# Performance work log

Measured on AMD Instinct MI355X. Metric: run time of the kernel, lower is better.

The kernel has to match this reference:

```python
import jax, jax.numpy as jnp
import numpy as np

D, ED, N, R, K, NL = 128, 256, 16, 8, 4, 3   # d_model, d_inner, d_state, dt_rank, d_conv, n_layers
B, L = 4, 1024
HID, OUT = 256, 2
EPS = 1e-5


def setup_inputs() -> dict:
    key = jax.random.key(0)
    ks = jax.random.split(key, 16)
    g = lambda k, shape, s=0.05: jax.random.normal(k, shape, dtype=jnp.float32) * s
    return {
        "x": jax.random.normal(ks[0], (B, L, D), dtype=jnp.float32),
        # Mamba params, stacked over (2 directions, NL layers)
        "rms_w": jnp.ones((2, NL, D), jnp.float32),
        "in_w": g(ks[1], (2, NL, 2 * ED, D)),
        "in_b": g(ks[2], (2, NL, 2 * ED)),
        "conv_w": g(ks[3], (2, NL, ED, K)),
        "conv_b": g(ks[4], (2, NL, ED)),
        "xproj_w": g(ks[5], (2, NL, R + 2 * N, ED)),
        "dt_w": g(ks[6], (2, NL, ED, R)),
        "dt_b": g(ks[7], (2, NL, ED)),
        "A_log": jnp.broadcast_to(jnp.log(jnp.arange(1.0, N + 1.0, dtype=jnp.float32)), (2, NL, ED, N)) + 0.0,
        "Dp": jnp.ones((2, NL, ED), jnp.float32),
        "out_w": g(ks[8], (2, NL, D, ED)),
        "out_b": g(ks[9], (2, NL, D)),
        # MLP head params (BatchNorm in training mode: batch stats)
        "bn1_g": jnp.ones((2 * D,), jnp.float32), "bn1_b": jnp.zeros((2 * D,), jnp.float32),
        "w1": g(ks[10], (HID, 2 * D)), "b1": g(ks[11], (HID,)),
        "bn2_g": jnp.ones((HID,), jnp.float32), "bn2_b": jnp.zeros((HID,), jnp.float32),
        "w2": g(ks[12], (HID, HID)), "b2": g(ks[13], (HID,)),
        "bn3_g": jnp.ones((HID,), jnp.float32), "bn3_b": jnp.zeros((HID,), jnp.float32),
        "w3": g(ks[14], (OUT, HID)), "b3": g(ks[15], (OUT,)),
    }


def _rms(x, w):
    return x * jax.lax.rsqrt(jnp.mean(x * x, axis=-1, keepdims=True) + EPS) * w


def _dwconv(x, w, b):
    # causal depthwise conv; x: (B,L,ED), w: (ED,K)
    y = jax.lax.conv_general_dilated(x.transpose(0, 2, 1), w[:, None, :], (1,), [(K - 1, 0)],
                                     feature_group_count=ED, dimension_numbers=("NCH", "OIH", "NCH"))
    return y.transpose(0, 2, 1) + b


def _ssm(dA, dBx, C):
    # dA,dBx: (B,L,ED,N); C: (B,L,N) -> y: (B,L,ED)
    def step(h, inp):
        a, bx, c = inp
        h = a * h + bx
        return h, jnp.einsum("ben,bn->be", h, c)
    h0 = jnp.zeros((dA.shape[0], ED, N), dA.dtype)
    _, ys = jax.lax.scan(step, h0, (dA.transpose(1, 0, 2, 3), dBx.transpose(1, 0, 2, 3), C.transpose(1, 0, 2)))
    return ys.transpose(1, 0, 2)


def _block(x, in_w, in_b, conv_w, conv_b, xproj_w, dt_w, dt_b, A_log, Dp, out_w, out_b):
    xz = x @ in_w.T + in_b
    xi, z = xz[..., :ED], xz[..., ED:]
    xi = jax.nn.silu(_dwconv(xi, conv_w, conv_b))
    dbc = xi @ xproj_w.T
    dt, Bm, Cm = dbc[..., :R], dbc[..., R:R + N], dbc[..., R + N:]
    delta = jax.nn.softplus(dt @ dt_w.T + dt_b)            # (B,L,ED)
    A = -jnp.exp(A_log)                                    # (ED,N)
    dA = jnp.exp(delta[..., None] * A)                     # (B,L,ED,N)
    dBx = (delta * xi)[..., None] * Bm[:, :, None, :]      # (B,L,ED,N)
    y = _ssm(dA, dBx, Cm) + Dp * xi
    y = y * jax.nn.silu(z)
    return y @ out_w.T + out_b


def _mamba(x, d, rms_w, in_w, in_b, conv_w, conv_b, xproj_w, dt_w, dt_b, A_log, Dp, out_w, out_b):
    for l in range(NL):
        x = x + _block(_rms(x, rms_w[d, l]), in_w[d, l], in_b[d, l], conv_w[d, l], conv_b[d, l],
                       xproj_w[d, l], dt_w[d, l], dt_b[d, l], A_log[d, l], Dp[d, l], out_w[d, l], out_b[d, l])
    return x


def _bn(x, g, b):
    m = jnp.mean(x, axis=0)
    v = jnp.mean((x - m) ** 2, axis=0)  # biased var, torch BN training mode
    return (x - m) * jax.lax.rsqrt(v + EPS) * g + b


def _forward(x, rms_w, in_w, in_b, conv_w, conv_b, xproj_w, dt_w, dt_b, A_log, Dp, out_w, out_b,
             bn1_g, bn1_b, w1, b1, bn2_g, bn2_b, w2, b2, bn3_g, bn3_b, w3, b3):
    mp = (rms_w, in_w, in_b, conv_w, conv_b, xproj_w, dt_w, dt_b, A_log, Dp, out_w, out_b)
    fwd = _mamba(x, 0, *mp)
    bwd = jnp.flip(_mamba(jnp.flip(x, axis=1), 1, *mp), axis=1)
    h = jnp.concatenate([fwd, bwd], axis=2).reshape(B * L, 2 * D)
    h = jax.nn.leaky_relu(_bn(h, bn1_g, bn1_b) @ w1.T + b1)
    h = jax.nn.leaky_relu(_bn(h, bn2_g, bn2_b) @ w2.T + b2)
    h = _bn(h, bn3_g, bn3_b) @ w3.T + b3
    return h.reshape(B, L, OUT)


def reference(x, rms_w, in_w, in_b, conv_w, conv_b, xproj_w, dt_w, dt_b, A_log, Dp, out_w, out_b,
              bn1_g, bn1_b, w1, b1, bn2_g, bn2_b, w2, b2, bn3_g, bn3_b, w3, b3):
    return _forward(x, rms_w, in_w, in_b, conv_w, conv_b, xproj_w, dt_w, dt_b, A_log, Dp, out_w, out_b,
                    bn1_g, bn1_b, w1, b1, bn2_g, bn2_b, w2, b2, bn3_g, bn3_b, w3, b3)
```

## Files before the change

### kernel.cpp

```cpp
#include <hip/hip_runtime.h>
#include <hip/hip_bf16.h>
#include <hip/hip_fp16.h>

#define NL 3
#define EPS 1e-5f

#define C_INB    393984L
#define C_CONVW  397056L
#define C_CONVB  403200L
#define C_XPROJW 404736L
#define C_DTW    466176L
#define C_DTB    478464L
#define C_ALOG   480000L
#define C_DP     504576L
#define C_OUTB   702720L
#define C_BN1G   703488L
#define C_BN1B   703744L
#define C_B1     769536L
#define C_BN2G   769792L
#define C_BN2B   770048L
#define C_B2     835840L
#define C_BN3G   836096L
#define C_BN3B   836352L
#define C_W3     836608L
#define C_B3     837120L
#define FLAG_OFF 837184L
#define X0_OFF   837248L
#define X1_OFF   1361536L
#define XZT_OFF  1885824L
#define DBCT_OFF 8177280L
#define YGP_OFF  8504960L
#define BNA_OFF  10603648L
#define HINW_OFF  10605184L
#define HOUTW_OFF 10801792L
#define HW1_OFF   10900096L
#define HW2_OFF   10932864L
#define HXW_OFF   10965632L
#define H1_OFF   XZT_OFF
#define H2_OFF   (XZT_OFF + 1048576L)

#define ASLD 68

struct Ptrs { const void* p[25]; };

typedef _Float16 half8 __attribute__((ext_vector_type(8)));
typedef float f32x4 __attribute__((ext_vector_type(4)));

static __device__ const int  CV_SRC[21] = {0,0,3,4,5,6,7,8,9,10,12,13,14,16,17,18,20,21,22,23,24};
static __device__ const long CV_DST[21] = {X0_OFF,X1_OFF,C_INB,C_CONVW,C_CONVB,C_XPROJW,C_DTW,C_DTB,C_ALOG,C_DP,
                                           C_OUTB,C_BN1G,C_BN1B,C_B1,C_BN2G,C_BN2B,C_B2,C_BN3G,C_BN3B,C_W3,C_B3};
static __device__ const int  CV_SZ[21]  = {524288,524288,3072,6144,1536,61440,12288,1536,24576,1536,
                                           768,256,256,256,256,256,256,256,256,512,2};

__device__ inline float ldsrc(const void* s, long i, bool isbf) {
  if (isbf) { unsigned int u = ((const unsigned short*)s)[i]; return __uint_as_float(u << 16); }
  return ((const float*)s)[i];
}

__global__ __launch_bounds__(256) void g_convert(Ptrs ps, float* __restrict__ ws) {
  bool isbf = (*(const unsigned int*)ps.p[1]) == 0x3F803F80u;
  int job = blockIdx.y;
  if (job == 0 && blockIdx.x == 0 && threadIdx.x == 0) ws[FLAG_OFF] = isbf ? 1.f : 0.f;
  int tid0 = blockIdx.x * 256 + threadIdx.x;
  int stride = gridDim.x * 256;
  if (job < 21) {
    int n = CV_SZ[job];
    const void* s = ps.p[CV_SRC[job]];
    float* dp = ws + CV_DST[job];
    bool permute = (job < 2);
    for (int i = tid0; i < n; i += stride) {
      long si = i;
      if (permute) {
        int row = i >> 7, col = i & 127;
        int b = row >> 10, p = row & 1023;
        int t = ((p & 63) << 4) + (p >> 6);
        si = ((long)((b << 10) + t) << 7) + col;
      }
      dp[i] = ldsrc(s, si, isbf);
    }
  } else if (job == 21) {
    _Float16* dp = (_Float16*)(ws + HINW_OFF);
    const void* sw = ps.p[2]; const void* sr = ps.p[1];
    for (int i = tid0; i < 393216; i += stride) {
      int dl = i >> 16, k = i & 127;
      dp[i] = (_Float16)(ldsrc(sw, i, isbf) * ldsrc(sr, dl*128 + k, isbf));
    }
  } else if (job == 22) {
    _Float16* dp = (_Float16*)(ws + HOUTW_OFF);
    const void* s = ps.p[11];
    for (int i = tid0; i < 196608; i += stride) dp[i] = (_Float16)ldsrc(s, i, isbf);
  } else if (job == 23) {
    _Float16* dp = (_Float16*)(ws + HW1_OFF);
    const void* s = ps.p[15];
    for (int i = tid0; i < 65536; i += stride) dp[i] = (_Float16)ldsrc(s, i, isbf);
  } else if (job == 24) {
    _Float16* dp = (_Float16*)(ws + HW2_OFF);
    const void* s = ps.p[19];
    for (int i = tid0; i < 65536; i += stride) dp[i] = (_Float16)ldsrc(s, i, isbf);
  } else if (job == 25) {
    for (int i = tid0; i < 1536; i += stride) ws[BNA_OFF + i] = 0.f;
  } else {
    _Float16* dp = (_Float16*)(ws + HXW_OFF);
    const void* s = ps.p[6];
    for (int i = tid0; i < 98304; i += stride) {
      int dl = i >> 14;
      int rem = i & 16383;
      int nn = rem >> 8, k = rem & 255;
      float v = (nn < 40) ? ldsrc(s, (long)(dl*40+nn)*256 + k, isbf) : 0.f;
      dp[i] = (_Float16)v;
    }
  }
}

__device__ inline void mm_inner(const float* As, const float* Bs, float4* acc) {
  int tx = threadIdx.x & 15, ty = threadIdx.x >> 4;
  #pragma unroll
  for (int k = 0; k < 64; ++k) {
    float4 av = *(const float4*)&As[k*ASLD + ty*4];
    float4 bv = *(const float4*)&Bs[k*ASLD + tx*4];
    acc[0].x = fmaf(av.x,bv.x,acc[0].x); acc[0].y = fmaf(av.x,bv.y,acc[0].y); acc[0].z = fmaf(av.x,bv.z,acc[0].z); acc[0].w = fmaf(av.x,bv.w,acc[0].w);
    acc[1].x = fmaf(av.y,bv.x,acc[1].x); acc[1].y = fmaf(av.y,bv.y,acc[1].y); acc[1].z = fmaf(av.y,bv.z,acc[1].z); acc[1].w = fmaf(av.y,bv.w,acc[1].w);
    acc[2].x = fmaf(av.z,bv.x,acc[2].x); acc[2].y = fmaf(av.z,bv.y,acc[2].y); acc[2].z = fmaf(av.z,bv.z,acc[2].z); acc[2].w = fmaf(av.z,bv.w,acc[2].w);
    acc[3].x = fmaf(av.w,bv.x,acc[3].x); acc[3].y = fmaf(av.w,bv.y,acc[3].y); acc[3].z = fmaf(av.w,bv.z,acc[3].z); acc[3].w = fmaf(av.w,bv.w,acc[3].w);
  }
}

__device__ inline void stageT_g(float* S, const float* src, int ld, int row0, int k0, int nvalid) {
  int m = threadIdx.x >> 2, q = threadIdx.x & 3;
  const float* p = src + (long)(row0 + m) * ld + k0 + q*16;
  bool ok = (row0 + m) < nvalid;
  #pragma unroll
  for (int j = 0; j < 4; ++j) {
    float4 v = ok ? *(const float4*)(p + j*4) : make_float4(0.f,0.f,0.f,0.f);
    int kk = q*16 + j*4;
    S[(kk+0)*ASLD+m] = v.x; S[(kk+1)*ASLD+m] = v.y; S[(kk+2)*ASLD+m] = v.z; S[(kk+3)*ASLD+m] = v.w;
  }
}

__device__ inline float softplusf(float x) {
  if (x > 20.f) return x;
  return __logf(1.f + __expf(x));
}
__device__ inline float siluf(float a) { return a / (1.f + __expf(-a)); }

__global__ __launch_bounds__(256) void g_k1m(float* __restrict__ ws, int layer) {
  int d = blockIdx.z, nt = blockIdx.y, pt = blockIdx.x;
  const float* X = ws + (d ? X1_OFF : X0_OFF);
  const _Float16* Wf = (const _Float16*)(ws + HINW_OFF) + (long)(d*NL+layer)*65536;
  const float* Bi = ws + C_INB + (d*NL+layer)*512;
  __shared__ float rsq[256];
  __shared__ float rsc[64];
  int p0 = pt*64;
  {
    int row = threadIdx.x >> 2, q = threadIdx.x & 3;
    const float* xp = X + (long)(p0+row)*128 + q*32;
    float s = 0.f;
    #pragma unroll
    for (int j = 0; j < 8; ++j) {
      float4 v = *(const float4*)(xp + j*4);
      s += v.x*v.x + v.y*v.y + v.z*v.z + v.w*v.w;
    }
    rsq[row*4+q] = s;
  }
  __syncthreads();
  if (threadIdx.x < 64) {
    float s = rsq[threadIdx.x*4] + rsq[threadIdx.x*4+1] + rsq[threadIdx.x*4+2] + rsq[threadIdx.x*4+3];
    rsc[threadIdx.x] = rsqrtf(s * (1.f/128.f) + EPS);
  }
  __syncthreads();
  int w = threadIdx.x >> 6, lane = threadIdx.x & 63;
  int quad = lane >> 4, lm = lane & 15;
  int n0 = nt*64 + w*16;
  f32x4 zero = {0.f,0.f,0.f,0.f};
  f32x4 acc[4] = {zero, zero, zero, zero};
  #pragma unroll
  for (int s = 0; s < 4; ++s) {
    int k0 = s*32 + quad*8;
    half8 af = *(const half8*)(Wf + (long)(n0+lm)*128 + k0);
    #pragma unroll
    for (int t = 0; t < 4; ++t) {
      int pr = t*16 + lm;
      const float* xp = X + (long)(p0+pr)*128 + k0;
      float4 v0 = *(const float4*)xp;
      float4 v1 = *(const float4*)(xp+4);
      float r = rsc[pr];
      half8 bf;
      bf[0]=(_Float16)(v0.x*r); bf[1]=(_Float16)(v0.y*r); bf[2]=(_Float16)(v0.z*r); bf[3]=(_Float16)(v0.w*r);
      bf[4]=(_Float16)(v1.x*r); bf[5]=(_Float16)(v1.y*r); bf[6]=(_Float16)(v1.z*r); bf[7]=(_Float16)(v1.w*r);
      acc[t] = __builtin_amdgcn_mfma_f32_16x16x32_f16(af, bf, acc[t], 0, 0, 0);
    }
  }
  float* xzt = ws + XZT_OFF + (long)d*2097152L;
  #pragma unroll
  for (int r = 0; r < 4; ++r) {
    int n = n0 + quad*4 + r;
    float bias = Bi[n];
    #pragma unroll
    for (int t = 0; t < 4; ++t) {
      int p = p0 + t*16 + lm;
      xzt[(long)n*4096 + p] = acc[t][r] + bias;
    }
  }
}

#define AHLD 264
__global__ __launch_bounds__(256) void g_k3m(float* __restrict__ ws, int layer) {
  int d = blockIdx.z, b = blockIdx.y;
  int ii = blockIdx.x >> 2, c0 = (blockIdx.x & 3) * 16;
  const float* xz = ws + XZT_OFF + (long)d*2097152L;
  const float* cw = ws + C_CONVW + (long)(d*NL+layer)*1024;
  const float* cbp = ws + C_CONVB + (d*NL+layer)*256;
  const _Float16* Wx = (const _Float16*)(ws + HXW_OFF) + (long)(d*NL+layer)*16384;
  __shared__ __align__(16) _Float16 Ah[16*AHLD];
  int col[4], sh[4];
  col[0] = ii; sh[0] = 0;
  #pragma unroll
  for (int j = 1; j < 4; ++j) {
    if (d == 0) { if (ii-j >= 0) { col[j]=ii-j; sh[j]=0; } else { col[j]=ii-j+16; sh[j]=-1; } }
    else        { if (ii+j <= 15){ col[j]=ii+j; sh[j]=0; } else { col[j]=ii+j-16; sh[j]=1; } }
  }
  int c = threadIdx.x & 15, eh = threadIdx.x >> 4;
  int gc = c0 + c;
  long rowbase = (long)b*1024;
  #pragma unroll 4
  for (int r = 0; r < 16; ++r) {
    int e = eh*16 + r;
    const float* xrow = xz + (long)e*4096 + rowbase;
    float4 cwv = *(const float4*)(cw + e*4);
    float v0 = xrow[col[0]*64 + gc];
    bool b1 = (sh[1] < 0 && gc == 0) || (sh[1] > 0 && gc == 63);
    bool b2 = (sh[2] < 0 && gc == 0) || (sh[2] > 0 && gc == 63);
    bool b3 = (sh[3] < 0 && gc == 0) || (sh[3] > 0 && gc == 63);
    float v1 = b1 ? 0.f : xrow[col[1]*64 + gc + sh[1]];
    float v2 = b2 ? 0.f : xrow[col[2]*64 + gc + sh[2]];
    float v3 = b3 ? 0.f : xrow[col[3]*64 + gc + sh[3]];
    float a = cbp[e] + cwv.w*v0 + cwv.z*v1 + cwv.y*v2 + cwv.x*v3;
    Ah[c*AHLD + e] = (_Float16)siluf(a);
  }
  __syncthreads();
  int w = threadIdx.x >> 6, lane = threadIdx.x & 63;
  int quad = lane >> 4, lm = lane & 15;
  f32x4 acc = {0.f,0.f,0.f,0.f};
  #pragma unroll
  for (int s = 0; s < 8; ++s) {
    int k0 = s*32 + quad*8;
    half8 af = *(const half8*)(Wx + (long)(w*16+lm)*256 + k0);
    half8 bf = *(const half8*)(&Ah[lm*AHLD + k0]);
    acc = __builtin_amdgcn_mfma_f32_16x16x32_f16(af, bf, acc, 0, 0, 0);
  }
  float* dbcT = ws + DBCT_OFF + (long)d*163840L;
  long P0 = (long)b*1024 + ii*64 + c0;
  #pragma unroll
  for (int r = 0; r < 4; ++r) {
    int n = w*16 + quad*4 + r;
    if (n < 40) dbcT[(long)n*4096 + P0 + lm] = acc[r];
  }
}

__global__ __launch_bounds__(256) void g_k5c(float* __restrict__ ws, int layer) {
  int d = blockIdx.z, b = blockIdx.y, eg = blockIdx.x;
  int es = threadIdx.x >> 6;
  int c  = threadIdx.x & 63;
  int e = eg*4 + es;
  int g0 = b*1024 + c;
  const float* xzrow = ws + XZT_OFF + (long)d*2097152L + (long)e*4096 + g0;
  const float* zp    = ws + XZT_OFF + (long)d*2097152L + (long)(256+e)*4096 + g0;
  const float* dbc = ws + DBCT_OFF + (long)d*163840L + g0;
  float*       yo  = ws + YGP_OFF + (long)d*1048576L + (long)e*4096 + g0;
  const float* dw = ws + C_DTW + (long)((d*NL+layer)*256 + e)*8;
  float dtb = ws[C_DTB + (d*NL+layer)*256 + e];
  const float* al = ws + C_ALOG + (long)((d*NL+layer)*256 + e)*16;
  float Dpe = ws[C_DP + (d*NL+layer)*256 + e];
  float4 cwv = *(const float4*)(ws + C_CONVW + (long)((d*NL+layer)*256 + e)*4);
  float cb = ws[C_CONVB + (d*NL+layer)*256 + e];
  float dtw[8];
  #pragma unroll
  for (int n = 0; n < 8; ++n) dtw[n] = dw[n];
  float Anv[16]; bool fast = true;
  #pragma unroll
  for (int n = 0; n < 16; ++n) {
    Anv[n] = -__expf(al[n]);
    fast = fast && (fabsf(Anv[n] + (float)(n+1)) < 1e-3f * (float)(n+1));
  }
  float w1, w2, w3;
  if (d == 0) {
    if (c > 0) { w1 = xzrow[959]; w2 = xzrow[895]; w3 = xzrow[831]; }
    else { w1 = w2 = w3 = 0.f; }
  } else {
    if (c < 63) { w1 = xzrow[1]; w2 = xzrow[65]; w3 = xzrow[129]; }
    else { w1 = w2 = w3 = 0.f; }
  }
  __shared__ float aL[4*64*17];
  __shared__ float hL[4*64*17];
  float h[16], ap[16], del[16], xcv[16];
  float Q = 1.f;
  #pragma unroll
  for (int n = 0; n < 16; ++n) { h[n] = 0.f; ap[n] = 1.f; }
  int i0 = d ? 15 : 0, di = d ? -1 : 1;
  for (int s = 0; s < 16; ++s) {
    int i = i0 + s*di;
    int off = i*64;
    float a0 = dtb;
    #pragma unroll
    for (int n = 0; n < 8; ++n) a0 += dbc[(long)n*4096 + off] * dtw[n];
    float dl = softplusf(a0);
    float xt = xzrow[off];
    float xc = siluf(cb + cwv.w*xt + cwv.z*w1 + cwv.y*w2 + cwv.x*w3);
    w3 = w2; w2 = w1; w1 = xt;
    del[s] = dl; xcv[s] = xc;
    float dx = dl * xc;
    if (fast) {
      float q = __expf(-dl);
      float qp[16];
      qp[0]=q; qp[1]=q*q; qp[2]=qp[1]*q; qp[3]=qp[1]*qp[1];
      float q4=qp[3];
      qp[4]=qp[0]*q4; qp[5]=qp[1]*q4; qp[6]=qp[2]*q4; qp[7]=q4*q4;
      float q8=qp[7];
      #pragma unroll
      for (int j = 0; j < 8; ++j) qp[8+j]=qp[j]*q8;
      Q *= q;
      #pragma unroll
      for (int n = 0; n < 16; ++n)
        h[n] = fmaf(qp[n], h[n], dx * dbc[(long)(8+n)*4096 + off]);
    } else {
      #pragma unroll
      for (int n = 0; n < 16; ++n) {
        float a = __expf(dl * Anv[n]);
        ap[n] *= a;
        h[n] = fmaf(a, h[n], dx * dbc[(long)(8+n)*4096 + off]);
      }
    }
  }
  if (fast) {
    float p = Q;
    #pragma unroll
    for (int n = 0; n < 16; ++n) { ap[n] = p; p *= Q; }
  }
  int base = (es*64 + c)*17;
  #pragma unroll
  for (int n = 0; n < 16; ++n) { aL[base+n] = ap[n]; hL[base+n] = h[n]; }
  __syncthreads();
  if (threadIdx.x < 64) {
    int e2 = threadIdx.x >> 4, n = threadIdx.x & 15;
    float h0 = 0.f;
    for (int s2 = 0; s2 < 64; ++s2) {
      int cc = d ? (63 - s2) : s2;
      int ix = (e2*64 + cc)*17 + n;
      float ta = aL[ix], th = hL[ix];
      aL[ix] = h0;
      h0 = fmaf(ta, h0, th);
    }
  }
  __syncthreads();
  #pragma unroll
  for (int n = 0; n < 16; ++n) h[n] = aL[base+n];
  for (int s = 0; s < 16; ++s) {
    int i = i0 + s*di;
    int off = i*64;
    float dl = del[s], xc = xcv[s];
    float dx = dl * xc;
    float zr = zp[off];
    float zg = zr / (1.f + __expf(-zr));
    float ya[4] = {0.f,0.f,0.f,0.f};
    if (fast) {
      float q = __expf(-dl);
      float qp[16];
      qp[0]=q; qp[1]=q*q; qp[2]=qp[1]*q; qp[3]=qp[1]*qp[1];
      float q4=qp[3];
      qp[4]=qp[0]*q4; qp[5]=qp[1]*q4; qp[6]=qp[2]*q4; qp[7]=q4*q4;
      float q8=qp[7];
      #pragma unroll
      for (int j = 0; j < 8; ++j) qp[8+j]=qp[j]*q8;
      #pragma unroll
      for (int n = 0; n < 16; ++n) {
        h[n] = fmaf(qp[n], h[n], dx * dbc[(long)(8+n)*4096 + off]);
        ya[n & 3] = fmaf(h[n], dbc[(long)(24+n)*4096 + off], ya[n & 3]);
      }
    } else {
      #pragma unroll
      for (int n = 0; n < 16; ++n) {
        float a = __expf(dl * Anv[n]);
        h[n] = fmaf(a, h[n], dx * dbc[(long)(8+n)*4096 + off]);
        ya[n & 3] = fmaf(h[n], dbc[(long)(24+n)*4096 + off], ya[n & 3]);
      }
    }
    float y = (ya[0] + ya[1]) + (ya[2] + ya[3]);
    y = fmaf(Dpe, xc, y);
    yo[off] = y * zg;
  }
}

__global__ __launch_bounds__(256) void g_k61(float* __restrict__ ws, int layer) {
  int d = blockIdx.z, pt = blockIdx.x;
  int p0 = pt*16;
  const float* Y = ws + YGP_OFF + (long)d*1048576L;
  const _Float16* Wf = (const _Float16*)(ws + HOUTW_OFF) + (long)(d*NL+layer)*32768;
  const float* Ob = ws + C_OUTB + (d*NL+layer)*128;
  float* Xd = ws + (d ? X1_OFF : X0_OFF);
  __shared__ __align__(16) _Float16 Ah[16*264];
  __shared__ float Xn[16*137];
  __shared__ float rsq[64];
  __shared__ float rsc[16];
  {
    int e = threadIdx.x;
    const float* yp = Y + (long)e*4096 + p0;
    float4 v0 = *(const float4*)yp;
    float4 v1 = *(const float4*)(yp+4);
    float4 v2 = *(const float4*)(yp+8);
    float4 v3 = *(const float4*)(yp+12);
    float vv[16] = {v0.x,v0.y,v0.z,v0.w, v1.x,v1.y,v1.z,v1.w,
                    v2.x,v2.y,v2.z,v2.w, v3.x,v3.y,v3.z,v3.w};
    #pragma unroll
    for (int p = 0; p < 16; ++p) Ah[p*264 + e] = (_Float16)vv[p];
  }
  __syncthreads();
  int w = threadIdx.x >> 6, lane = threadIdx.x & 63;
  int quad = lane >> 4, lm = lane & 15;
  f32x4 zero = {0.f,0.f,0.f,0.f};
  f32x4 acc[2] = {zero, zero};
  #pragma unroll
  for (int s = 0; s < 8; ++s) {
    int k0 = s*32 + quad*8;
    half8 af = *(const half8*)(&Ah[lm*264 + k0]);
    #pragma unroll
    for (int t = 0; t < 2; ++t) {
      int n = w*32 + t*16 + lm;
      half8 bf = *(const half8*)(Wf + (long)n*256 + k0);
      acc[t] = __builtin_amdgcn_mfma_f32_16x16x32_f16(af, bf, acc[t], 0, 0, 0);
    }
  }
  bool dostats = (layer == NL-1);
  float* bna = ws + BNA_OFF;
  #pragma unroll
  for (int t = 0; t < 2; ++t) {
    int n = w*32 + t*16 + lm;
    float ob = Ob[n];
    float s1 = 0.f, s2 = 0.f;
    #pragma unroll
    for (int r = 0; r < 4; ++r) {
      int p = p0 + quad*4 + r;
      float v = acc[t][r] + ob + Xd[(long)p*128 + n];
      Xd[(long)p*128 + n] = v;
      Xn[(quad*4 + r)*137 + n] = v;
      s1 += v; s2 += v*v;
    }
    if (dostats) {
      s1 += __shfl_xor(s1, 16, 64); s2 += __shfl_xor(s2, 16, 64);
      s1 += __shfl_xor(s1, 32, 64); s2 += __shfl_xor(s2, 32, 64);
      if (quad == 0) {
        int ch = d*128 + n;
        atomicAdd(&bna[ch], s1);
        atomicAdd(&bna[256 + ch], s2);
      }
    }
  }
  if (layer == NL-1) return;
  __syncthreads();
  if (threadIdx.x < 64) {
    int pl = threadIdx.x >> 2, qq = threadIdx.x & 3;
    float s = 0.f;
    const float* xr = &Xn[pl*137 + qq*32];
    #pragma unroll
    for (int k = 0; k < 32; ++k) s += xr[k]*xr[k];
    rsq[threadIdx.x] = s;
  }
  __syncthreads();
  if (threadIdx.x < 16) {
    float s = rsq[threadIdx.x*4] + rsq[threadIdx.x*4+1] + rsq[threadIdx.x*4+2] + rsq[threadIdx.x*4+3];
    rsc[threadIdx.x] = rsqrtf(s * (1.f/128.f) + EPS);
  }
  __syncthreads();
  const _Float16* Wn = (const _Float16*)(ws + HINW_OFF) + (long)(d*NL+layer+1)*65536;
  const float* Bi = ws + C_INB + (d*NL+layer+1)*512;
  f32x4 acc2[8] = {zero,zero,zero,zero,zero,zero,zero,zero};
  float r = rsc[lm];
  #pragma unroll
  for (int s = 0; s < 4; ++s) {
    int k0 = s*32 + quad*8;
    half8 bf;
    const float* xr = &Xn[lm*137 + k0];
    #pragma unroll
    for (int j = 0; j < 8; ++j) bf[j] = (_Float16)(xr[j] * r);
    #pragma unroll
    for (int tt = 0; tt < 8; ++tt) {
      int n2 = w*128 + tt*16 + lm;
      half8 af = *(const half8*)(Wn + (long)n2*128 + k0);
      acc2[tt] = __builtin_amdgcn_mfma_f32_16x16x32_f16(af, bf, acc2[tt], 0, 0, 0);
    }
  }
  float* xzt = ws + XZT_OFF + (long)d*2097152L;
  #pragma unroll
  for (int tt = 0; tt < 8; ++tt) {
    #pragma unroll
    for (int rr = 0; rr < 4; ++rr) {
      int n2 = w*128 + tt*16 + quad*4 + rr;
      xzt[(long)n2*4096 + p0 + lm] = acc2[tt][rr] + Bi[n2];
    }
  }
}

template<int STAGE>
__global__ __launch_bounds__(256) void g_hgm(float* __restrict__ ws) {
  int p0 = blockIdx.x * 16;
  __shared__ float scL[256], shL[256];
  {
    int k = threadIdx.x;
    float S = ws[BNA_OFF + STAGE*512 + k], S2 = ws[BNA_OFF + STAGE*512 + 256 + k];
    float mean = S * (1.f/4096.f);
    float var = S2 * (1.f/4096.f) - mean*mean;
    const float* g = ws + (STAGE == 0 ? C_BN1G : C_BN2G);
    const float* bb = ws + (STAGE == 0 ? C_BN1B : C_BN2B);
    float sc = g[k] * rsqrtf(var + EPS);
    scL[k] = sc; shL[k] = bb[k] - mean*sc;
  }
  __syncthreads();
  const _Float16* Wf = (const _Float16*)(ws + (STAGE == 0 ? HW1_OFF : HW2_OFF));
  const float* bias = ws + (STAGE == 0 ? C_B1 : C_B2);
  float* H = ws + (STAGE == 0 ? H1_OFF : H2_OFF);
  int w = threadIdx.x >> 6, lane = threadIdx.x & 63;
  int quad = lane >> 4, lm = lane & 15;
  f32x4 zero = {0.f,0.f,0.f,0.f};
  f32x4 acc[4] = {zero, zero, zero, zero};
  #pragma unroll
  for (int s = 0; s < 8; ++s) {
    int k0 = s*32 + quad*8;
    const float* src;
    if (STAGE == 0) src = (k0 < 128) ? (ws + X0_OFF + (long)(p0+lm)*128 + k0)
                                     : (ws + X1_OFF + (long)(p0+lm)*128 + (k0-128));
    else            src = ws + H1_OFF + (long)(p0+lm)*256 + k0;
    float4 v0 = *(const float4*)src, v1 = *(const float4*)(src+4);
    float4 c0 = *(const float4*)&scL[k0], c1 = *(const float4*)&scL[k0+4];
    float4 h0 = *(const float4*)&shL[k0], h1 = *(const float4*)&shL[k0+4];
    half8 af;
    af[0]=(_Float16)(v0.x*c0.x+h0.x); af[1]=(_Float16)(v0.y*c0.y+h0.y);
    af[2]=(_Float16)(v0.z*c0.z+h0.z); af[3]=(_Float16)(v0.w*c0.w+h0.w);
    af[4]=(_Float16)(v1.x*c1.x+h1.x); af[5]=(_Float16)(v1.y*c1.y+h1.y);
    af[6]=(_Float16)(v1.z*c1.z+h1.z); af[7]=(_Float16)(v1.w*c1.w+h1.w);
    #pragma unroll
    for (int t = 0; t < 4; ++t) {
      int n = w*64 + t*16 + lm;
      half8 bf = *(const half8*)(Wf + (long)n*256 + k0);
      acc[t] = __builtin_amdgcn_mfma_f32_16x16x32_f16(af, bf, acc[t], 0, 0, 0);
    }
  }
  float* bna = ws + BNA_OFF + (STAGE+1)*512;
  #pragma unroll
  for (int t = 0; t < 4; ++t) {
    int n = w*64 + t*16 + lm;
    float bs = bias[n];
    float s1 = 0.f, s2 = 0.f;
    #pragma unroll
    for (int r = 0; r < 4; ++r) {
      int p = p0 + quad*4 + r;
      float v = acc[t][r] + bs;
      v = v > 0.f ? v : 0.01f*v;
      H[(long)p*256 + n] = v;
      s1 += v; s2 += v*v;
    }
    s1 += __shfl_xor(s1, 16, 64); s2 += __shfl_xor(s2, 16, 64);
    s1 += __shfl_xor(s1, 32, 64); s2 += __shfl_xor(s2, 32, 64);
    if (quad == 0) {
      atomicAdd(&bna[n], s1);
      atomicAdd(&bna[256 + n], s2);
    }
  }
}

__global__ __launch_bounds__(256) void g_hg2(float* __restrict__ ws, void* dout) {
  int mt = blockIdx.x;
  __shared__ float As[64*ASLD];
  __shared__ float Bs[64*ASLD];
  __shared__ float scL[256], shL[256];
  {
    int k = threadIdx.x;
    float S = ws[BNA_OFF + 2*512 + k], S2 = ws[BNA_OFF + 2*512 + 256 + k];
    float mean = S * (1.f/4096.f);
    float var = S2 * (1.f/4096.f) - mean*mean;
    float sc = ws[C_BN3G + k] * rsqrtf(var + EPS);
    scL[k] = sc; shL[k] = ws[C_BN3B + k] - mean*sc;
  }
  __syncthreads();
  float4 acc[4] = {make_float4(0,0,0,0),make_float4(0,0,0,0),make_float4(0,0,0,0),make_float4(0,0,0,0)};
  for (int kt = 0; kt < 4; ++kt) {
    int k0 = kt * 64;
    {
      int m = threadIdx.x >> 2, q = threadIdx.x & 3;
      const float* p = ws + H2_OFF + (long)(mt*64 + m)*256 + k0 + q*16;
      #pragma unroll
      for (int j = 0; j < 4; ++j) {
        float4 v  = *(const float4*)(p + j*4);
        float4 s4 = *(const float4*)&scL[k0 + q*16 + j*4];
        float4 h4 = *(const float4*)&shL[k0 + q*16 + j*4];
        int kk = q*16 + j*4;
        As[(kk+0)*ASLD+m] = v.x*s4.x + h4.x; As[(kk+1)*ASLD+m] = v.y*s4.y + h4.y;
        As[(kk+2)*ASLD+m] = v.z*s4.z + h4.z; As[(kk+3)*ASLD+m] = v.w*s4.w + h4.w;
      }
    }
    stageT_g(Bs, ws + C_W3, 256, 0, k0, 2);
    __syncthreads();
    mm_inner(As, Bs, acc);
    __syncthreads();
  }
  int tx = threadIdx.x & 15, ty = threadIdx.x >> 4;
  if (tx == 0) {
    bool isbf = ws[FLAG_OFF] != 0.f;
    float b0 = ws[C_B3], b1 = ws[C_B3 + 1];
    #pragma unroll
    for (int i = 0; i < 4; ++i) {
      int r = mt*64 + ty*4 + i;
      int b = r >> 10, p = r & 1023;
      int t = ((p & 63) << 4) + (p >> 6);
      long tok = (long)(b << 10) + t;
      float v0 = acc[i].x + b0, v1 = acc[i].y + b1;
      if (isbf) {
        __hip_bfloat16* o = (__hip_bfloat16*)dout;
        o[tok*2]   = __float2bfloat16(v0);
        o[tok*2+1] = __float2bfloat16(v1);
      } else {
        float* o = (float*)dout;
        o[tok*2] = v0; o[tok*2+1] = v1;
      }
    }
  }
}

extern "C" void kernel_launch(void* const* d_in, const int* in_sizes, int n_in,
                              void* d_out, int out_size, void* d_ws, size_t ws_size,
                              hipStream_t stream) {
  (void)in_sizes; (void)n_in; (void)out_size; (void)ws_size;
  float* ws = (float*)d_ws;
  Ptrs ps;
  for (int i = 0; i < 25; ++i) ps.p[i] = d_in[i];
  g_convert<<<dim3(32, 27), dim3(256), 0, stream>>>(ps, ws);
  g_k1m<<<dim3(64, 8, 2), dim3(256), 0, stream>>>(ws, 0);
  for (int l = 0; l < NL; ++l) {
    g_k3m<<<dim3(64, 4, 2), dim3(256), 0, stream>>>(ws, l);
    g_k5c<<<dim3(64, 4, 2), dim3(256), 0, stream>>>(ws, l);
    g_k61<<<dim3(256, 1, 2), dim3(256), 0, stream>>>(ws, l);
  }
  g_hgm<0><<<dim3(256), dim3(256), 0, stream>>>(ws);
  g_hgm<1><<<dim3(256), dim3(256), 0, stream>>>(ws);
  g_hg2<<<dim3(64), dim3(256), 0, stream>>>(ws, d_out);
}
```

Measured before the change: 388.8 us.

## Split SSM scan state dimension across two waves per channel

The selective-scan kernel now assigns each inner channel to two wavefronts, each handling 8 of the 16 state elements. The grid is doubled and each block covers 2 channels instead of 4. Partial y contributions are combined through shared memory before gating and the store. This raises parallelism and cuts per-thread registers, in exchange for duplicated delta/conv computation, extra shared-memory traffic and syncs, and idle half-waves during the final output loop.

```diff
diff --git a/kernel.cpp b/kernel.cpp
--- a/kernel.cpp
+++ b/kernel.cpp
@@ -257,11 +257,12 @@
   }
 }
 
-__global__ __launch_bounds__(256) void g_k5c(float* __restrict__ ws, int layer) {
+__global__ __launch_bounds__(256) void g_k5n(float* __restrict__ ws, int layer) {
   int d = blockIdx.z, b = blockIdx.y, eg = blockIdx.x;
-  int es = threadIdx.x >> 6;
+  int w = threadIdx.x >> 6;
+  int es = w >> 1, nh = w & 1;
   int c  = threadIdx.x & 63;
-  int e = eg*4 + es;
+  int e = eg*2 + es;
   int g0 = b*1024 + c;
   const float* xzrow = ws + XZT_OFF + (long)d*2097152L + (long)e*4096 + g0;
   const float* zp    = ws + XZT_OFF + (long)d*2097152L + (long)(256+e)*4096 + g0;
@@ -269,18 +270,19 @@
   float*       yo  = ws + YGP_OFF + (long)d*1048576L + (long)e*4096 + g0;
   const float* dw = ws + C_DTW + (long)((d*NL+layer)*256 + e)*8;
   float dtb = ws[C_DTB + (d*NL+layer)*256 + e];
-  const float* al = ws + C_ALOG + (long)((d*NL+layer)*256 + e)*16;
+  const float* al = ws + C_ALOG + (long)((d*NL+layer)*256 + e)*16 + nh*8;
   float Dpe = ws[C_DP + (d*NL+layer)*256 + e];
   float4 cwv = *(const float4*)(ws + C_CONVW + (long)((d*NL+layer)*256 + e)*4);
   float cb = ws[C_CONVB + (d*NL+layer)*256 + e];
   float dtw[8];
   #pragma unroll
   for (int n = 0; n < 8; ++n) dtw[n] = dw[n];
-  float Anv[16]; bool fast = true;
-  #pragma unroll
-  for (int n = 0; n < 16; ++n) {
+  float Anv[8]; bool fast = true;
+  #pragma unroll
+  for (int n = 0; n < 8; ++n) {
     Anv[n] = -__expf(al[n]);
-    fast = fast && (fabsf(Anv[n] + (float)(n+1)) < 1e-3f * (float)(n+1));
+    float ni = (float)(nh*8 + n + 1);
+    fast = fast && (fabsf(Anv[n] + ni) < 1e-3f * ni);
   }
   float w1, w2, w3;
   if (d == 0) {
@@ -290,13 +292,14 @@
     if (c < 63) { w1 = xzrow[1]; w2 = xzrow[65]; w3 = xzrow[129]; }
     else { w1 = w2 = w3 = 0.f; }
   }
-  __shared__ float aL[4*64*17];
-  __shared__ float hL[4*64*17];
-  float h[16], ap[16], del[16], xcv[16];
+  __shared__ float aL[2*64*17];
+  __shared__ float hL[2*64*17];
+  float h[8], ap[8], del[16], xcv[16];
   float Q = 1.f;
   #pragma unroll
-  for (int n = 0; n < 16; ++n) { h[n] = 0.f; ap[n] = 1.f; }
+  for (int n = 0; n < 8; ++n) { h[n] = 0.f; ap[n] = 1.f; }
   int i0 = d ? 15 : 0, di = d ? -1 : 1;
+  long nb = (long)(8 + nh*8) * 4096;
   for (int s = 0; s < 16; ++s) {
     int i = i0 + s*di;
     int off = i*64;
@@ -311,36 +314,47 @@
     float dx = dl * xc;
     if (fast) {
       float q = __expf(-dl);
-      float qp[16];
-      qp[0]=q; qp[1]=q*q; qp[2]=qp[1]*q; qp[3]=qp[1]*qp[1];
-      float q4=qp[3];
-      qp[4]=qp[0]*q4; qp[5]=qp[1]*q4; qp[6]=qp[2]*q4; qp[7]=q4*q4;
-      float q8=qp[7];
-      #pragma unroll
-      for (int j = 0; j < 8; ++j) qp[8+j]=qp[j]*q8;
+      float qb[8];
+      qb[0]=q; qb[1]=q*q; qb[2]=qb[1]*q; qb[3]=qb[1]*qb[1];
+      qb[4]=qb[3]*q; qb[5]=qb[3]*qb[1]; qb[6]=qb[3]*qb[2]; qb[7]=qb[3]*qb[3];
+      float qp[8];
+      if (nh) { float q8 = qb[7];
+        #pragma unroll
+        for (int j = 0; j < 8; ++j) qp[j] = qb[j]*q8;
+      } else {
+        #pragma unroll
+        for (int j = 0; j < 8; ++j) qp[j] = qb[j];
+      }
       Q *= q;
       #pragma unroll
-      for (int n = 0; n < 16; ++n)
-        h[n] = fmaf(qp[n], h[n], dx * dbc[(long)(8+n)*4096 + off]);
+      for (int n = 0; n < 8; ++n)
+        h[n] = fmaf(qp[n], h[n], dx * dbc[nb + (long)n*4096 + off]);
     } else {
       #pragma unroll
-      for (int n = 0; n < 16; ++n) {
+      for (int n = 0; n < 8; ++n) {
         float a = __expf(dl * Anv[n]);
         ap[n] *= a;
-        h[n] = fmaf(a, h[n], dx * dbc[(long)(8+n)*4096 + off]);
+        h[n] = fmaf(a, h[n], dx * dbc[nb + (long)n*4096 + off]);
       }
     }
   }
   if (fast) {
-    float p = Q;
-    #pragma unroll
-    for (int n = 0; n < 16; ++n) { ap[n] = p; p *= Q; }
-  }
-  int base = (es*64 + c)*17;
-  #pragma unroll
-  for (int n = 0; n < 16; ++n) { aL[base+n] = ap[n]; hL[base+n] = h[n]; }
-  __syncthreads();
-  if (threadIdx.x < 64) {
+    float Qb[8];
+    Qb[0]=Q; Qb[1]=Q*Q; Qb[2]=Qb[1]*Q; Qb[3]=Qb[1]*Qb[1];
+    Qb[4]=Qb[3]*Q; Qb[5]=Qb[3]*Qb[1]; Qb[6]=Qb[3]*Qb[2]; Qb[7]=Qb[3]*Qb[3];
+    if (nh) { float Q8 = Qb[7];
+      #pragma unroll
+      for (int n = 0; n < 8; ++n) ap[n] = Qb[n]*Q8;
+    } else {
+      #pragma unroll
+      for (int n = 0; n < 8; ++n) ap[n] = Qb[n];
+    }
+  }
+  int base = (es*64 + c)*17 + nh*8;
+  #pragma unroll
+  for (int n = 0; n < 8; ++n) { aL[base+n] = ap[n]; hL[base+n] = h[n]; }
+  __syncthreads();
+  if (threadIdx.x < 32) {
     int e2 = threadIdx.x >> 4, n = threadIdx.x & 15;
     float h0 = 0.f;
     for (int s2 = 0; s2 < 64; ++s2) {
@@ -353,40 +367,60 @@
   }
   __syncthreads();
   #pragma unroll
-  for (int n = 0; n < 16; ++n) h[n] = aL[base+n];
+  for (int n = 0; n < 8; ++n) h[n] = aL[base+n];
+  float ya[16];
+  long cbn = (long)(24 + nh*8) * 4096;
   for (int s = 0; s < 16; ++s) {
     int i = i0 + s*di;
     int off = i*64;
-    float dl = del[s], xc = xcv[s];
-    float dx = dl * xc;
-    float zr = zp[off];
-    float zg = zr / (1.f + __expf(-zr));
-    float ya[4] = {0.f,0.f,0.f,0.f};
+    float dl = del[s];
+    float dx = dl * xcv[s];
+    float y8 = 0.f;
     if (fast) {
       float q = __expf(-dl);
-      float qp[16];
-      qp[0]=q; qp[1]=q*q; qp[2]=qp[1]*q; qp[3]=qp[1]*qp[1];
-      float q4=qp[3];
-      qp[4]=qp[0]*q4; qp[5]=qp[1]*q4; qp[6]=qp[2]*q4; qp[7]=q4*q4;
-      float q8=qp[7];
+      float qb[8];
+      qb[0]=q; qb[1]=q*q; qb[2]=qb[1]*q; qb[3]=qb[1]*qb[1];
+      qb[4]=qb[3]*q; qb[5]=qb[3]*qb[1]; qb[6]=qb[3]*qb[2]; qb[7]=qb[3]*qb[3];
+      float qp[8];
+      if (nh) { float q8 = qb[7];
+        #pragma unroll
+        for (int j = 0; j < 8; ++j) qp[j] = qb[j]*q8;
+      } else {
+        #pragma unroll
+        for (int j = 0; j < 8; ++j) qp[j] = qb[j];
+      }
       #pragma unroll
-      for (int j = 0; j < 8; ++j) qp[8+j]=qp[j]*q8;
-      #pragma unroll
-      for (int n = 0; n < 16; ++n) {
-        h[n] = fmaf(qp[n], h[n], dx * dbc[(long)(8+n)*4096 + off]);
-        ya[n & 3] = fmaf(h[n], dbc[(long)(24+n)*4096 + off], ya[n & 3]);
+      for (int n = 0; n < 8; ++n) {
+        h[n] = fmaf(qp[n], h[n], dx * dbc[nb + (long)n*4096 + off]);
+        y8 = fmaf(h[n], dbc[cbn + (long)n*4096 + off], y8);
       }
     } else {
       #pragma unroll
-      for (int n = 0; n < 16; ++n) {
+      for (int n = 0; n < 8; ++n) {
         float a = __expf(dl * Anv[n]);
-        h[n] = fmaf(a, h[n], dx * dbc[(long)(8+n)*4096 + off]);
-        ya[n & 3] = fmaf(h[n], dbc[(long)(24+n)*4096 + off], ya[n & 3]);
-      }
-    }
-    float y = (ya[0] + ya[1]) + (ya[2] + ya[3]);
-    y = fmaf(Dpe, xc, y);
-    yo[off] = y * zg;
+        h[n] = fmaf(a, h[n], dx * dbc[nb + (long)n*4096 + off]);
+        y8 = fmaf(h[n], dbc[cbn + (long)n*4096 + off], y8);
+      }
+    }
+    ya[s] = y8;
+  }
+  __syncthreads();
+  if (nh == 1) {
+    int yb = (es*64 + c)*17;
+    #pragma unroll
+    for (int s = 0; s < 16; ++s) hL[yb + s] = ya[s];
+  }
+  __syncthreads();
+  if (nh == 0) {
+    int yb = (es*64 + c)*17;
+    for (int s = 0; s < 16; ++s) {
+      int i = i0 + s*di;
+      int off = i*64;
+      float zr = zp[off];
+      float zg = zr / (1.f + __expf(-zr));
+      float y = ya[s] + hL[yb + s] + Dpe * xcv[s];
+      yo[off] = y * zg;
+    }
   }
 }
 
@@ -635,7 +669,7 @@
   g_k1m<<<dim3(64, 8, 2), dim3(256), 0, stream>>>(ws, 0);
   for (int l = 0; l < NL; ++l) {
     g_k3m<<<dim3(64, 4, 2), dim3(256), 0, stream>>>(ws, l);
-    g_k5c<<<dim3(64, 4, 2), dim3(256), 0, stream>>>(ws, l);
+    g_k5n<<<dim3(128, 4, 2), dim3(256), 0, stream>>>(ws, l);
     g_k61<<<dim3(256, 1, 2), dim3(256), 0, stream>>>(ws, l);
   }
   g_hgm<0><<<dim3(256), dim3(256), 0, stream>>>(ws);
```

Result: slower. 463.3 us (+19.2%).

## Split selective scan into 8-step chunks with two channels per block

Applied to the files above, without the earlier changes.

The chunked SSM scan kernel now assigns 2 channels per block instead of 4, and each thread handles an 8-timestep chunk instead of 16. This doubles the grid to 128 blocks along x, so each thread has a shorter serial recurrence and more threads run in parallel. The cost is a longer serial cross-chunk combine: 128 chunks per channel instead of 64, done by only 32 threads. The index mapping for the token layout and the conv halo reads are rewritten to match the new chunk assignment.

```diff
diff --git a/kernel.cpp b/kernel.cpp
--- a/kernel.cpp
+++ b/kernel.cpp
@@ -257,16 +257,17 @@
   }
 }
 
-__global__ __launch_bounds__(256) void g_k5c(float* __restrict__ ws, int layer) {
+__global__ __launch_bounds__(256) void g_k5d(float* __restrict__ ws, int layer) {
   int d = blockIdx.z, b = blockIdx.y, eg = blockIdx.x;
-  int es = threadIdx.x >> 6;
-  int c  = threadIdx.x & 63;
-  int e = eg*4 + es;
-  int g0 = b*1024 + c;
-  const float* xzrow = ws + XZT_OFF + (long)d*2097152L + (long)e*4096 + g0;
-  const float* zp    = ws + XZT_OFF + (long)d*2097152L + (long)(256+e)*4096 + g0;
-  const float* dbc = ws + DBCT_OFF + (long)d*163840L + g0;
-  float*       yo  = ws + YGP_OFF + (long)d*1048576L + (long)e*4096 + g0;
+  int tid = threadIdx.x;
+  int es = tid >> 7;
+  int rem = tid & 127;
+  int half = rem >> 6, m = rem & 63;
+  int e = eg*2 + es;
+  const float* xb = ws + XZT_OFF + (long)d*2097152L + (long)e*4096 + b*1024;
+  const float* zb = ws + XZT_OFF + (long)d*2097152L + (long)(256+e)*4096 + b*1024;
+  const float* db = ws + DBCT_OFF + (long)d*163840L + b*1024;
+  float*       yb = ws + YGP_OFF + (long)d*1048576L + (long)e*4096 + b*1024;
   const float* dw = ws + C_DTW + (long)((d*NL+layer)*256 + e)*8;
   float dtb = ws[C_DTB + (d*NL+layer)*256 + e];
   const float* al = ws + C_ALOG + (long)((d*NL+layer)*256 + e)*16;
@@ -282,29 +283,35 @@
     Anv[n] = -__expf(al[n]);
     fast = fast && (fabsf(Anv[n] + (float)(n+1)) < 1e-3f * (float)(n+1));
   }
+  int tf = (m << 4) + (half << 3);
   float w1, w2, w3;
+  #define PADDR(t) ((((t) & 15) << 6) + ((t) >> 4))
   if (d == 0) {
-    if (c > 0) { w1 = xzrow[959]; w2 = xzrow[895]; w3 = xzrow[831]; }
-    else { w1 = w2 = w3 = 0.f; }
+    w1 = (tf >= 1) ? xb[PADDR(tf-1)] : 0.f;
+    w2 = (tf >= 2) ? xb[PADDR(tf-2)] : 0.f;
+    w3 = (tf >= 3) ? xb[PADDR(tf-3)] : 0.f;
   } else {
-    if (c < 63) { w1 = xzrow[1]; w2 = xzrow[65]; w3 = xzrow[129]; }
-    else { w1 = w2 = w3 = 0.f; }
-  }
-  __shared__ float aL[4*64*17];
-  __shared__ float hL[4*64*17];
-  float h[16], ap[16], del[16], xcv[16];
+    int tl = tf + 7;
+    w1 = (tl <= 1022) ? xb[PADDR(tl+1)] : 0.f;
+    w2 = (tl <= 1021) ? xb[PADDR(tl+2)] : 0.f;
+    w3 = (tl <= 1020) ? xb[PADDR(tl+3)] : 0.f;
+  }
+  #undef PADDR
+  __shared__ float aL[2*128*17];
+  __shared__ float hL[2*128*17];
+  float h[16], ap[16], del[8], xcv[8];
   float Q = 1.f;
   #pragma unroll
   for (int n = 0; n < 16; ++n) { h[n] = 0.f; ap[n] = 1.f; }
-  int i0 = d ? 15 : 0, di = d ? -1 : 1;
-  for (int s = 0; s < 16; ++s) {
+  int i0 = d ? 7 : 0, di = d ? -1 : 1;
+  for (int s = 0; s < 8; ++s) {
     int i = i0 + s*di;
-    int off = i*64;
+    int off = ((half << 3) + i) << 6;
     float a0 = dtb;
     #pragma unroll
-    for (int n = 0; n < 8; ++n) a0 += dbc[(long)n*4096 + off] * dtw[n];
+    for (int n = 0; n < 8; ++n) a0 += db[(long)n*4096 + off + m] * dtw[n];
     float dl = softplusf(a0);
-    float xt = xzrow[off];
+    float xt = xb[off + m];
     float xc = siluf(cb + cwv.w*xt + cwv.z*w1 + cwv.y*w2 + cwv.x*w3);
     w3 = w2; w2 = w1; w1 = xt;
     del[s] = dl; xcv[s] = xc;
@@ -321,13 +328,13 @@
       Q *= q;
       #pragma unroll
       for (int n = 0; n < 16; ++n)
-        h[n] = fmaf(qp[n], h[n], dx * dbc[(long)(8+n)*4096 + off]);
+        h[n] = fmaf(qp[n], h[n], dx * db[(long)(8+n)*4096 + off + m]);
     } else {
       #pragma unroll
       for (int n = 0; n < 16; ++n) {
         float a = __expf(dl * Anv[n]);
         ap[n] *= a;
-        h[n] = fmaf(a, h[n], dx * dbc[(long)(8+n)*4096 + off]);
+        h[n] = fmaf(a, h[n], dx * db[(long)(8+n)*4096 + off + m]);
       }
     }
   }
@@ -336,16 +343,17 @@
     #pragma unroll
     for (int n = 0; n < 16; ++n) { ap[n] = p; p *= Q; }
   }
-  int base = (es*64 + c)*17;
+  int chunk = (m << 1) + half;
+  int base = (es*128 + chunk)*17;
   #pragma unroll
   for (int n = 0; n < 16; ++n) { aL[base+n] = ap[n]; hL[base+n] = h[n]; }
   __syncthreads();
-  if (threadIdx.x < 64) {
-    int e2 = threadIdx.x >> 4, n = threadIdx.x & 15;
+  if (tid < 32) {
+    int e2 = tid >> 4, n = tid & 15;
     float h0 = 0.f;
-    for (int s2 = 0; s2 < 64; ++s2) {
-      int cc = d ? (63 - s2) : s2;
-      int ix = (e2*64 + cc)*17 + n;
+    for (int s2 = 0; s2 < 128; ++s2) {
+      int cc = d ? (127 - s2) : s2;
+      int ix = (e2*128 + cc)*17 + n;
       float ta = aL[ix], th = hL[ix];
       aL[ix] = h0;
       h0 = fmaf(ta, h0, th);
@@ -354,12 +362,12 @@
   __syncthreads();
   #pragma unroll
   for (int n = 0; n < 16; ++n) h[n] = aL[base+n];
-  for (int s = 0; s < 16; ++s) {
+  for (int s = 0; s < 8; ++s) {
     int i = i0 + s*di;
-    int off = i*64;
+    int off = ((half << 3) + i) << 6;
     float dl = del[s], xc = xcv[s];
     float dx = dl * xc;
-    float zr = zp[off];
+    float zr = zb[off + m];
     float zg = zr / (1.f + __expf(-zr));
     float ya[4] = {0.f,0.f,0.f,0.f};
     if (fast) {
@@ -373,20 +381,20 @@
       for (int j = 0; j < 8; ++j) qp[8+j]=qp[j]*q8;
       #pragma unroll
       for (int n = 0; n < 16; ++n) {
-        h[n] = fmaf(qp[n], h[n], dx * dbc[(long)(8+n)*4096 + off]);
-        ya[n & 3] = fmaf(h[n], dbc[(long)(24+n)*4096 + off], ya[n & 3]);
+        h[n] = fmaf(qp[n], h[n], dx * db[(long)(8+n)*4096 + off + m]);
+        ya[n & 3] = fmaf(h[n], db[(long)(24+n)*4096 + off + m], ya[n & 3]);
       }
     } else {
       #pragma unroll
       for (int n = 0; n < 16; ++n) {
         float a = __expf(dl * Anv[n]);
-        h[n] = fmaf(a, h[n], dx * dbc[(long)(8+n)*4096 + off]);
-        ya[n & 3] = fmaf(h[n], dbc[(long)(24+n)*4096 + off], ya[n & 3]);
+        h[n] = fmaf(a, h[n], dx * db[(long)(8+n)*4096 + off + m]);
+        ya[n & 3] = fmaf(h[n], db[(long)(24+n)*4096 + off + m], ya[n & 3]);
       }
     }
     float y = (ya[0] + ya[1]) + (ya[2] + ya[3]);
     y = fmaf(Dpe, xc, y);
-    yo[off] = y * zg;
+    yb[off + m] = y * zg;
   }
 }
 
@@ -635,7 +643,7 @@
   g_k1m<<<dim3(64, 8, 2), dim3(256), 0, stream>>>(ws, 0);
   for (int l = 0; l < NL; ++l) {
     g_k3m<<<dim3(64, 4, 2), dim3(256), 0, stream>>>(ws, l);
-    g_k5c<<<dim3(64, 4, 2), dim3(256), 0, stream>>>(ws, l);
+    g_k5d<<<dim3(128, 4, 2), dim3(256), 0, stream>>>(ws, l);
     g_k61<<<dim3(256, 1, 2), dim3(256), 0, stream>>>(ws, l);
   }
   g_hgm<0><<<dim3(256), dim3(256), 0, stream>>>(ws);
```

Measured after the change: 461.9 us. 1.19x slower.

## Replace LDS sequential chunk-carry scan with wavefront shuffle parallel scan

Applied to the files above, without the earlier changes.

Swaps the shared-memory serial carry propagation across the 64 chunks for a Kogge-Stone prefix scan using wave shuffles. Each thread combines the (decay, state) pairs in log2(64) steps, then shifts the result by one to get an exclusive carry-in. This removes two block barriers, the LDS traffic, and a 64-step serial loop run by only one wave. In exchange every thread does more shuffle and FMA work per state.

```diff
diff --git a/kernel.cpp b/kernel.cpp
--- a/kernel.cpp
+++ b/kernel.cpp
@@ -257,7 +257,7 @@
   }
 }
 
-__global__ __launch_bounds__(256) void g_k5c(float* __restrict__ ws, int layer) {
+__global__ __launch_bounds__(256) void g_k5w(float* __restrict__ ws, int layer) {
   int d = blockIdx.z, b = blockIdx.y, eg = blockIdx.x;
   int es = threadIdx.x >> 6;
   int c  = threadIdx.x & 63;
@@ -290,8 +290,6 @@
     if (c < 63) { w1 = xzrow[1]; w2 = xzrow[65]; w3 = xzrow[129]; }
     else { w1 = w2 = w3 = 0.f; }
   }
-  __shared__ float aL[4*64*17];
-  __shared__ float hL[4*64*17];
   float h[16], ap[16], del[16], xcv[16];
   float Q = 1.f;
   #pragma unroll
@@ -336,24 +334,24 @@
     #pragma unroll
     for (int n = 0; n < 16; ++n) { ap[n] = p; p *= Q; }
   }
-  int base = (es*64 + c)*17;
-  #pragma unroll
-  for (int n = 0; n < 16; ++n) { aL[base+n] = ap[n]; hL[base+n] = h[n]; }
-  __syncthreads();
-  if (threadIdx.x < 64) {
-    int e2 = threadIdx.x >> 4, n = threadIdx.x & 15;
-    float h0 = 0.f;
-    for (int s2 = 0; s2 < 64; ++s2) {
-      int cc = d ? (63 - s2) : s2;
-      int ix = (e2*64 + cc)*17 + n;
-      float ta = aL[ix], th = hL[ix];
-      aL[ix] = h0;
-      h0 = fmaf(ta, h0, th);
-    }
-  }
-  __syncthreads();
-  #pragma unroll
-  for (int n = 0; n < 16; ++n) h[n] = aL[base+n];
+  #pragma unroll
+  for (int n = 0; n < 16; ++n) {
+    float A = ap[n], B = h[n];
+    #pragma unroll
+    for (int off = 1; off < 64; off <<= 1) {
+      float Ap, Bp; bool valid;
+      if (d == 0) { Ap = __shfl_up(A, off, 64);  Bp = __shfl_up(B, off, 64);  valid = (c >= off); }
+      else        { Ap = __shfl_down(A, off, 64); Bp = __shfl_down(B, off, 64); valid = (c + off < 64); }
+      float Bn = fmaf(A, Bp, B);
+      float An = A * Ap;
+      B = valid ? Bn : B;
+      A = valid ? An : A;
+    }
+    float h0;
+    if (d == 0) { h0 = __shfl_up(B, 1, 64);  if (c == 0)  h0 = 0.f; }
+    else        { h0 = __shfl_down(B, 1, 64); if (c == 63) h0 = 0.f; }
+    h[n] = h0;
+  }
   for (int s = 0; s < 16; ++s) {
     int i = i0 + s*di;
     int off = i*64;
@@ -635,7 +633,7 @@
   g_k1m<<<dim3(64, 8, 2), dim3(256), 0, stream>>>(ws, 0);
   for (int l = 0; l < NL; ++l) {
     g_k3m<<<dim3(64, 4, 2), dim3(256), 0, stream>>>(ws, l);
-    g_k5c<<<dim3(64, 4, 2), dim3(256), 0, stream>>>(ws, l);
+    g_k5w<<<dim3(64, 4, 2), dim3(256), 0, stream>>>(ws, l);
     g_k61<<<dim3(256, 1, 2), dim3(256), 0, stream>>>(ws, l);
   }
   g_hgm<0><<<dim3(256), dim3(256), 0, stream>>>(ws);
```

Measured after the change: 424.1 us. +9.1%, slower.
